# Kernel optimization log

Hardware: AMD Instinct MI355X
Metric: run time of the kernel (lower is better)

The kernel has to match this reference:

```python
import jax, jax.numpy as jnp
import numpy as np

HEAD_SIZE = 64
EMBED_DIM = 1024

def setup_inputs() -> dict:
    key = jax.random.key(0)
    kx, kq, kk, kv = jax.random.split(key, 4)
    B, T, C, H = 8, 2048, EMBED_DIM, HEAD_SIZE
    scale = 1.0 / np.sqrt(C)
    x = jax.random.normal(kx, (B, T, C), dtype=jnp.float32)
    # nn.Linear(C, H, bias=False): weight (H, C); store as (C, H) for x @ W
    Wq = jax.random.normal(kq, (C, H), dtype=jnp.float32) * scale
    Wk = jax.random.normal(kk, (C, H), dtype=jnp.float32) * scale
    Wv = jax.random.normal(kv, (C, H), dtype=jnp.float32) * scale
    return {"x": x, "Wq": Wq, "Wk": Wk, "Wv": Wv}

def reference(x, Wq, Wk, Wv):
    B, T, C = x.shape
    H = Wq.shape[1]
    q = x @ Wq  # (B, T, H)
    k = x @ Wk
    v = x @ Wv
    # scaled scores with causal mask (tril)
    wei = jnp.einsum('bth,bsh->bts', q, k) * (H ** -0.5)  # (B, T, T)
    causal = jnp.tril(jnp.ones((T, T), dtype=bool))
    wei = jnp.where(causal, wei, -jnp.inf)
    wei = jax.nn.softmax(wei, axis=-1)
    out = jnp.einsum('bts,bsh->bth', wei, v)  # (B, T, H)
    return out
```

## Files before the change

kernel.cpp:

```cpp
#include <hip/hip_runtime.h>

#define T_SEQ 2048
#define C_DIM 1024
#define H_DIM 64
#define B_DIM 8
#define NROW (B_DIM * T_SEQ)

typedef __attribute__((ext_vector_type(8))) short short8;
typedef __attribute__((ext_vector_type(4))) float f32x4;

__device__ __forceinline__ short f2bf(float f) {
  unsigned u = __builtin_bit_cast(unsigned, f);
  u += 0x7fffu + ((u >> 16) & 1u);
  return (short)(u >> 16);
}

__global__ __launch_bounds__(256) void w_transpose(
    const float* __restrict__ Wq, const float* __restrict__ Wk,
    const float* __restrict__ Wv, short* __restrict__ Wt) {
  __shared__ float tile[64][65];
  const int mat = blockIdx.x >> 4;
  const int k0 = (blockIdx.x & 15) * 64;
  const float* W = (mat == 0) ? Wq : (mat == 1 ? Wk : Wv);
  const int t = threadIdx.x;
#pragma unroll
  for (int i = 0; i < 16; ++i) {
    int idx = t + i * 256;
    int kk = idx >> 6, h = idx & 63;
    tile[kk][h] = W[(size_t)(k0 + kk) * H_DIM + h];
  }
  __syncthreads();
#pragma unroll
  for (int i = 0; i < 16; ++i) {
    int idx = t + i * 256;
    int h = idx >> 6, kk = idx & 63;
    Wt[((size_t)mat * 64 + h) * C_DIM + k0 + kk] = f2bf(tile[kk][h]);
  }
}

__device__ __forceinline__ int lds_addr(int tile, int kh, int qd, int nn) {
  return tile * 2048 + kh * 512 + (qd * 16 + (nn ^ ((kh * 4 + qd) & 7))) * 8;
}

__global__ __launch_bounds__(256) void qkv_gemm(
    const float* __restrict__ x, const short* __restrict__ Wt,
    short* __restrict__ q, short* __restrict__ k, short* __restrict__ vt) {
  __shared__ __align__(16) short As[4096];
  __shared__ __align__(16) short Bs[24576];
  const int tid = threadIdx.x;
  const int w = tid >> 6, lane = tid & 63;
  const int n16 = lane & 15, quad = lane >> 4;
  const int row0 = blockIdx.x * 32;

  f32x4 acc[2][3];
#pragma unroll
  for (int mt = 0; mt < 2; ++mt)
#pragma unroll
    for (int ln = 0; ln < 3; ++ln) acc[mt][ln] = (f32x4){0.f, 0.f, 0.f, 0.f};

  short8 bstg[12];
  float4 astg[2][2];

#pragma unroll
  for (int i = 0; i < 12; ++i) {
    const int u = i * 256 + tid, h = u >> 4, uk = u & 15;
    bstg[i] = *(const short8*)(Wt + (size_t)h * C_DIM + uk * 8);
  }
#pragma unroll
  for (int i = 0; i < 2; ++i) {
    const int u2 = i * 256 + tid, sr = u2 >> 4, f = u2 & 15;
    const float* ap = x + (size_t)(row0 + sr) * C_DIM + f * 8;
    astg[i][0] = *(const float4*)ap;
    astg[i][1] = *(const float4*)(ap + 4);
  }

  for (int kc = 0; kc < 8; ++kc) {
    __syncthreads();
#pragma unroll
    for (int i = 0; i < 12; ++i) {
      const int u = i * 256 + tid, h = u >> 4, uk = u & 15;
      *(short8*)(Bs + lds_addr(h >> 4, uk >> 2, uk & 3, h & 15)) = bstg[i];
    }
#pragma unroll
    for (int i = 0; i < 2; ++i) {
      const int u2 = i * 256 + tid, sr = u2 >> 4, f = u2 & 15;
      short8 av;
#pragma unroll
      for (int e = 0; e < 4; ++e) {
        av[e] = f2bf(((const float*)&astg[i][0])[e]);
        av[e + 4] = f2bf(((const float*)&astg[i][1])[e]);
      }
      *(short8*)(As + lds_addr(sr >> 4, f >> 2, f & 3, sr & 15)) = av;
    }
    __syncthreads();
    if (kc < 7) {
      const int k0n = (kc + 1) * 128;
#pragma unroll
      for (int i = 0; i < 12; ++i) {
        const int u = i * 256 + tid, h = u >> 4, uk = u & 15;
        bstg[i] = *(const short8*)(Wt + (size_t)h * C_DIM + k0n + uk * 8);
      }
#pragma unroll
      for (int i = 0; i < 2; ++i) {
        const int u2 = i * 256 + tid, sr = u2 >> 4, f = u2 & 15;
        const float* ap = x + (size_t)(row0 + sr) * C_DIM + k0n + f * 8;
        astg[i][0] = *(const float4*)ap;
        astg[i][1] = *(const float4*)(ap + 4);
      }
    }
#pragma unroll
    for (int kh = 0; kh < 4; ++kh) {
      short8 afr[2];
#pragma unroll
      for (int mt = 0; mt < 2; ++mt)
        afr[mt] = *(const short8*)(As + lds_addr(mt, kh, quad, n16));
#pragma unroll
      for (int ln = 0; ln < 3; ++ln) {
        const short8 bfr =
            *(const short8*)(Bs + lds_addr(w * 3 + ln, kh, quad, n16));
        acc[0][ln] =
            __builtin_amdgcn_mfma_f32_16x16x32_bf16(afr[0], bfr, acc[0][ln], 0, 0, 0);
        acc[1][ln] =
            __builtin_amdgcn_mfma_f32_16x16x32_bf16(afr[1], bfr, acc[1][ln], 0, 0, 0);
      }
    }
  }

  const int b = row0 >> 11;
#pragma unroll
  for (int mt = 0; mt < 2; ++mt)
#pragma unroll
    for (int ln = 0; ln < 3; ++ln) {
      const int ntg = w * 3 + ln;
      const int mat = ntg >> 2;
      const int cl = (ntg & 3) * 16 + n16;
#pragma unroll
      for (int r = 0; r < 4; ++r) {
        const int row = row0 + mt * 16 + quad * 4 + r;
        const float v = acc[mt][ln][r];
        if (mat == 0)
          q[(size_t)row * H_DIM + cl] = f2bf(v * 0.125f);
        else if (mat == 1)
          k[(size_t)row * H_DIM + cl] = f2bf(v);
        else
          vt[((size_t)b * H_DIM + cl) * T_SEQ + (row & (T_SEQ - 1))] = f2bf(v);
      }
    }
}

__global__ __launch_bounds__(256) void attn_mfma(
    const short* __restrict__ q, const short* __restrict__ k,
    const short* __restrict__ vt, float* __restrict__ out) {
  __shared__ __align__(16) short pbuf[4][1024];
  __shared__ __align__(16) float oshare[3][1024];
  __shared__ __align__(16) float lshare[3][256];
  const int tid = threadIdx.x;
  const int w = tid >> 6;
  const int lane = tid & 63;
  const int n16 = lane & 15, quad = lane >> 4;
  const int b = blockIdx.x & 7;
  const int qt = (T_SEQ / 16 - 1) - (blockIdx.x >> 3);
  const int r0 = qt * 16;

  const short* qb = q + ((size_t)b * T_SEQ + r0) * H_DIM;
  const short* kb = k + (size_t)b * T_SEQ * H_DIM;
  const short* vb = vt + (size_t)b * H_DIM * T_SEQ;

  const short8 aq0 = *(const short8*)(qb + (size_t)n16 * H_DIM + quad * 8);
  const short8 aq1 = *(const short8*)(qb + (size_t)n16 * H_DIM + 32 + quad * 8);

  f32x4 O[4];
#pragma unroll
  for (int i = 0; i < 4; ++i) O[i] = (f32x4){0.f, 0.f, 0.f, 0.f};
  float lsum[4] = {0.f, 0.f, 0.f, 0.f};

  const int nj = (r0 + 16 + 63) >> 6;
  for (int jt = w; jt < nj; jt += 4) {
    const int j0 = jt * 64;

    short8 bk[4][2];
#pragma unroll
    for (int nt = 0; nt < 4; ++nt) {
      const short* kp = kb + (size_t)(j0 + nt * 16 + n16) * H_DIM + quad * 8;
      bk[nt][0] = *(const short8*)kp;
      bk[nt][1] = *(const short8*)(kp + 32);
    }

    f32x4 s[4];
#pragma unroll
    for (int nt = 0; nt < 4; ++nt) {
      f32x4 z = (f32x4){0.f, 0.f, 0.f, 0.f};
      z = __builtin_amdgcn_mfma_f32_16x16x32_bf16(aq0, bk[nt][0], z, 0, 0, 0);
      z = __builtin_amdgcn_mfma_f32_16x16x32_bf16(aq1, bk[nt][1], z, 0, 0, 0);
      s[nt] = z;
    }

    const bool full = (j0 + 64 <= r0);
#pragma unroll
    for (int nt = 0; nt < 4; ++nt) {
      const int base =
          (nt >> 1) * 512 + ((((nt & 1) << 1) | (n16 >> 3)) * 128) + (n16 & 7);
#pragma unroll
      for (int r = 0; r < 4; ++r) {
        float p;
        if (full) {
          p = __expf(s[nt][r]);
        } else {
          const int j = j0 + nt * 16 + n16;
          const int row = r0 + quad * 4 + r;
          p = (j <= row) ? __expf(s[nt][r]) : 0.f;
        }
        lsum[r] += p;
        pbuf[w][base + (quad * 4 + r) * 8] = f2bf(p);
      }
    }

    short8 bv[4][2];
#pragma unroll
    for (int ht = 0; ht < 4; ++ht)
#pragma unroll
      for (int kh = 0; kh < 2; ++kh)
        bv[ht][kh] = *(const short8*)(vb + (size_t)(ht * 16 + n16) * T_SEQ +
                                      j0 + kh * 32 + quad * 8);

    const short8 ap0 = *(const short8*)(&pbuf[w][0] + lane * 8);
    const short8 ap1 = *(const short8*)(&pbuf[w][0] + 512 + lane * 8);

#pragma unroll
    for (int ht = 0; ht < 4; ++ht) {
      O[ht] = __builtin_amdgcn_mfma_f32_16x16x32_bf16(ap0, bv[ht][0], O[ht], 0, 0, 0);
      O[ht] = __builtin_amdgcn_mfma_f32_16x16x32_bf16(ap1, bv[ht][1], O[ht], 0, 0, 0);
    }
  }

  if (w != 0) {
#pragma unroll
    for (int ht = 0; ht < 4; ++ht)
#pragma unroll
      for (int r = 0; r < 4; ++r)
        oshare[w - 1][(ht * 4 + r) * 64 + lane] = O[ht][r];
#pragma unroll
    for (int r = 0; r < 4; ++r) lshare[w - 1][r * 64 + lane] = lsum[r];
  }
  __syncthreads();
  if (w == 0) {
#pragma unroll
    for (int ht = 0; ht < 4; ++ht)
#pragma unroll
      for (int r = 0; r < 4; ++r) {
        float a = O[ht][r];
#pragma unroll
        for (int ow = 0; ow < 3; ++ow) a += oshare[ow][(ht * 4 + r) * 64 + lane];
        O[ht][r] = a;
      }
#pragma unroll
    for (int r = 0; r < 4; ++r) {
      float vsum = lsum[r];
#pragma unroll
      for (int ow = 0; ow < 3; ++ow) vsum += lshare[ow][r * 64 + lane];
      vsum += __shfl_xor(vsum, 1);
      vsum += __shfl_xor(vsum, 2);
      vsum += __shfl_xor(vsum, 4);
      vsum += __shfl_xor(vsum, 8);
      lsum[r] = vsum;
    }
#pragma unroll
    for (int ht = 0; ht < 4; ++ht)
#pragma unroll
      for (int r = 0; r < 4; ++r)
        out[((size_t)b * T_SEQ + r0 + quad * 4 + r) * H_DIM + ht * 16 + n16] =
            O[ht][r] / lsum[r];
  }
}

extern "C" void kernel_launch(void* const* d_in, const int* in_sizes, int n_in,
                              void* d_out, int out_size, void* d_ws,
                              size_t ws_size, hipStream_t stream) {
  const float* x = (const float*)d_in[0];
  const float* Wq = (const float*)d_in[1];
  const float* Wk = (const float*)d_in[2];
  const float* Wv = (const float*)d_in[3];

  char* ws = (char*)d_ws;
  short* Wt = (short*)ws;
  short* q = (short*)(ws + 3 * 64 * 1024 * 2);
  short* kk = (short*)(ws + 3 * 64 * 1024 * 2 + 2097152);
  short* vt = (short*)(ws + 3 * 64 * 1024 * 2 + 2 * 2097152);

  w_transpose<<<48, 256, 0, stream>>>(Wq, Wk, Wv, Wt);
  qkv_gemm<<<NROW / 32, 256, 0, stream>>>(x, Wt, q, kk, vt);
  attn_mfma<<<B_DIM * (T_SEQ / 16), 256, 0, stream>>>(q, kk, vt, (float*)d_out);
}
```

Baseline: 143.3 us.

## Share K tiles in LDS across four query-row waves per block

Each block now handles 64 query rows, one 16-row slice per wave, instead of splitting the key range of 16 rows across waves. K tiles are staged cooperatively into swizzled LDS with register prefetch of the next tile, so all four waves reuse them. This removes the cross-wave O/lsum reduction through shared memory. The log2(e) factor is folded into the Q scale so exp2f replaces __expf. The cost is two block-wide barriers per key tile, a quarter as many blocks, and V reads that are still per-wave from global memory.

```diff
diff --git a/kernel.cpp b/kernel.cpp
--- a/kernel.cpp
+++ b/kernel.cpp
@@ -127,6 +127,7 @@
   }
 
   const int b = row0 >> 11;
+  const float QSCALE = 0.1803368801111137f;
 #pragma unroll
   for (int mt = 0; mt < 2; ++mt)
 #pragma unroll
@@ -139,7 +140,7 @@
         const int row = row0 + mt * 16 + quad * 4 + r;
         const float v = acc[mt][ln][r];
         if (mat == 0)
-          q[(size_t)row * H_DIM + cl] = f2bf(v * 0.125f);
+          q[(size_t)row * H_DIM + cl] = f2bf(v * QSCALE);
         else if (mat == 1)
           k[(size_t)row * H_DIM + cl] = f2bf(v);
         else
@@ -151,51 +152,75 @@
 __global__ __launch_bounds__(256) void attn_mfma(
     const short* __restrict__ q, const short* __restrict__ k,
     const short* __restrict__ vt, float* __restrict__ out) {
+  __shared__ __align__(16) short Ks[64 * 64];
   __shared__ __align__(16) short pbuf[4][1024];
-  __shared__ __align__(16) float oshare[3][1024];
-  __shared__ __align__(16) float lshare[3][256];
   const int tid = threadIdx.x;
-  const int w = tid >> 6;
-  const int lane = tid & 63;
+  const int w = tid >> 6, lane = tid & 63;
   const int n16 = lane & 15, quad = lane >> 4;
   const int b = blockIdx.x & 7;
-  const int qt = (T_SEQ / 16 - 1) - (blockIdx.x >> 3);
-  const int r0 = qt * 16;
-
-  const short* qb = q + ((size_t)b * T_SEQ + r0) * H_DIM;
+  const int qb = 31 - (blockIdx.x >> 3);
+  const int row0 = qb * 64;
+  const int r0w = row0 + w * 16;
+
+  const short* qp = q + ((size_t)b * T_SEQ + r0w) * H_DIM;
   const short* kb = k + (size_t)b * T_SEQ * H_DIM;
   const short* vb = vt + (size_t)b * H_DIM * T_SEQ;
 
-  const short8 aq0 = *(const short8*)(qb + (size_t)n16 * H_DIM + quad * 8);
-  const short8 aq1 = *(const short8*)(qb + (size_t)n16 * H_DIM + 32 + quad * 8);
+  const short8 aq0 = *(const short8*)(qp + (size_t)n16 * H_DIM + quad * 8);
+  const short8 aq1 = *(const short8*)(qp + (size_t)n16 * H_DIM + 32 + quad * 8);
 
   f32x4 O[4];
 #pragma unroll
   for (int i = 0; i < 4; ++i) O[i] = (f32x4){0.f, 0.f, 0.f, 0.f};
   float lsum[4] = {0.f, 0.f, 0.f, 0.f};
 
-  const int nj = (r0 + 16 + 63) >> 6;
-  for (int jt = w; jt < nj; jt += 4) {
+  short8 kst[2];
+#pragma unroll
+  for (int i = 0; i < 2; ++i) {
+    const int g = i * 256 + tid, row = g >> 3, u = g & 7;
+    kst[i] = *(const short8*)(kb + (size_t)row * H_DIM + u * 8);
+  }
+
+  for (int jt = 0; jt <= qb; ++jt) {
     const int j0 = jt * 64;
-
-    short8 bk[4][2];
+    __syncthreads();
+#pragma unroll
+    for (int i = 0; i < 2; ++i) {
+      const int g = i * 256 + tid, row = g >> 3, u = g & 7;
+      *(short8*)(Ks + row * 64 + (u ^ (row & 7)) * 8) = kst[i];
+    }
+    __syncthreads();
+
+    short8 bv[4][2];
+#pragma unroll
+    for (int ht = 0; ht < 4; ++ht)
+#pragma unroll
+      for (int kh = 0; kh < 2; ++kh)
+        bv[ht][kh] = *(const short8*)(vb + (size_t)(ht * 16 + n16) * T_SEQ +
+                                      j0 + kh * 32 + quad * 8);
+    if (jt < qb) {
+#pragma unroll
+      for (int i = 0; i < 2; ++i) {
+        const int g = i * 256 + tid, row = g >> 3, u = g & 7;
+        kst[i] =
+            *(const short8*)(kb + (size_t)(j0 + 64 + row) * H_DIM + u * 8);
+      }
+    }
+
+    f32x4 s[4];
 #pragma unroll
     for (int nt = 0; nt < 4; ++nt) {
-      const short* kp = kb + (size_t)(j0 + nt * 16 + n16) * H_DIM + quad * 8;
-      bk[nt][0] = *(const short8*)kp;
-      bk[nt][1] = *(const short8*)(kp + 32);
-    }
-
-    f32x4 s[4];
-#pragma unroll
-    for (int nt = 0; nt < 4; ++nt) {
+      const int j = nt * 16 + n16;
+      const short8 bk0 = *(const short8*)(Ks + j * 64 + (quad ^ (j & 7)) * 8);
+      const short8 bk1 =
+          *(const short8*)(Ks + j * 64 + ((4 + quad) ^ (j & 7)) * 8);
       f32x4 z = (f32x4){0.f, 0.f, 0.f, 0.f};
-      z = __builtin_amdgcn_mfma_f32_16x16x32_bf16(aq0, bk[nt][0], z, 0, 0, 0);
-      z = __builtin_amdgcn_mfma_f32_16x16x32_bf16(aq1, bk[nt][1], z, 0, 0, 0);
+      z = __builtin_amdgcn_mfma_f32_16x16x32_bf16(aq0, bk0, z, 0, 0, 0);
+      z = __builtin_amdgcn_mfma_f32_16x16x32_bf16(aq1, bk1, z, 0, 0, 0);
       s[nt] = z;
     }
 
-    const bool full = (j0 + 64 <= r0);
+    const bool full = (jt != qb);
 #pragma unroll
     for (int nt = 0; nt < 4; ++nt) {
       const int base =
@@ -204,25 +229,17 @@
       for (int r = 0; r < 4; ++r) {
         float p;
         if (full) {
-          p = __expf(s[nt][r]);
+          p = exp2f(s[nt][r]);
         } else {
           const int j = j0 + nt * 16 + n16;
-          const int row = r0 + quad * 4 + r;
-          p = (j <= row) ? __expf(s[nt][r]) : 0.f;
+          const int row = r0w + quad * 4 + r;
+          p = (j <= row) ? exp2f(s[nt][r]) : 0.f;
         }
         lsum[r] += p;
         pbuf[w][base + (quad * 4 + r) * 8] = f2bf(p);
       }
     }
 
-    short8 bv[4][2];
-#pragma unroll
-    for (int ht = 0; ht < 4; ++ht)
-#pragma unroll
-      for (int kh = 0; kh < 2; ++kh)
-        bv[ht][kh] = *(const short8*)(vb + (size_t)(ht * 16 + n16) * T_SEQ +
-                                      j0 + kh * 32 + quad * 8);
-
     const short8 ap0 = *(const short8*)(&pbuf[w][0] + lane * 8);
     const short8 ap1 = *(const short8*)(&pbuf[w][0] + 512 + lane * 8);
 
@@ -233,44 +250,22 @@
     }
   }
 
-  if (w != 0) {
-#pragma unroll
-    for (int ht = 0; ht < 4; ++ht)
-#pragma unroll
-      for (int r = 0; r < 4; ++r)
-        oshare[w - 1][(ht * 4 + r) * 64 + lane] = O[ht][r];
-#pragma unroll
-    for (int r = 0; r < 4; ++r) lshare[w - 1][r * 64 + lane] = lsum[r];
-  }
-  __syncthreads();
-  if (w == 0) {
-#pragma unroll
-    for (int ht = 0; ht < 4; ++ht)
-#pragma unroll
-      for (int r = 0; r < 4; ++r) {
-        float a = O[ht][r];
-#pragma unroll
-        for (int ow = 0; ow < 3; ++ow) a += oshare[ow][(ht * 4 + r) * 64 + lane];
-        O[ht][r] = a;
-      }
-#pragma unroll
-    for (int r = 0; r < 4; ++r) {
-      float vsum = lsum[r];
-#pragma unroll
-      for (int ow = 0; ow < 3; ++ow) vsum += lshare[ow][r * 64 + lane];
-      vsum += __shfl_xor(vsum, 1);
-      vsum += __shfl_xor(vsum, 2);
-      vsum += __shfl_xor(vsum, 4);
-      vsum += __shfl_xor(vsum, 8);
-      lsum[r] = vsum;
-    }
-#pragma unroll
-    for (int ht = 0; ht < 4; ++ht)
-#pragma unroll
-      for (int r = 0; r < 4; ++r)
-        out[((size_t)b * T_SEQ + r0 + quad * 4 + r) * H_DIM + ht * 16 + n16] =
-            O[ht][r] / lsum[r];
-  }
+#pragma unroll
+  for (int r = 0; r < 4; ++r) {
+    float vsum = lsum[r];
+    vsum += __shfl_xor(vsum, 1);
+    vsum += __shfl_xor(vsum, 2);
+    vsum += __shfl_xor(vsum, 4);
+    vsum += __shfl_xor(vsum, 8);
+    lsum[r] = vsum;
+  }
+
+#pragma unroll
+  for (int ht = 0; ht < 4; ++ht)
+#pragma unroll
+    for (int r = 0; r < 4; ++r)
+      out[((size_t)b * T_SEQ + r0w + quad * 4 + r) * H_DIM + ht * 16 + n16] =
+          O[ht][r] / lsum[r];
 }
 
 extern "C" void kernel_launch(void* const* d_in, const int* in_sizes, int n_in,
@@ -289,5 +284,5 @@
 
   w_transpose<<<48, 256, 0, stream>>>(Wq, Wk, Wv, Wt);
   qkv_gemm<<<NROW / 32, 256, 0, stream>>>(x, Wt, q, kk, vt);
-  attn_mfma<<<B_DIM * (T_SEQ / 16), 256, 0, stream>>>(q, kk, vt, (float*)d_out);
-}
+  attn_mfma<<<B_DIM * (T_SEQ / 64), 256, 0, stream>>>(q, kk, vt, (float*)d_out);
+}
```

Measured after the change: 153.3 us. 1.07x slower.
